# Kernel optimization log

Hardware: AMD Instinct MI355X
Metric: run time of the kernel (lower is better)

## Reference

```python
import jax, jax.numpy as jnp
import numpy as np

B, N, E = 4, 1024, 8192
NF_IN, NF_H, NF_OUT = 32, 128, 3


def _lin(key, fan_in, fan_out):
    k1, k2 = jax.random.split(key)
    bound = 1.0 / np.sqrt(fan_in)
    W = jax.random.uniform(k1, (fan_in, fan_out), jnp.float32, -bound, bound)
    b = jax.random.uniform(k2, (fan_out,), jnp.float32, -bound, bound)
    return W, b


def setup_inputs() -> dict:
    key = jax.random.key(0)
    ks = jax.random.split(key, 16)
    x = jax.random.normal(ks[0], (B, N, NF_IN), jnp.float32)
    # One-hot receiver/sender relation matrices [B, E, N]
    recv = jax.random.randint(ks[1], (B, E), 0, N)
    send = jax.random.randint(ks[2], (B, E), 0, N)
    Rr = jax.nn.one_hot(recv, N, dtype=jnp.float32)
    Rs = jax.nn.one_hot(send, N, dtype=jnp.float32)
    neW0, neb0 = _lin(ks[3], NF_IN, NF_H)
    neW1, neb1 = _lin(ks[4], NF_H, NF_H)
    neW2, neb2 = _lin(ks[5], NF_H, NF_H)
    eeW0, eeb0 = _lin(ks[6], NF_IN * 2, NF_H)
    eeW1, eeb1 = _lin(ks[7], NF_H, NF_H)
    eeW2, eeb2 = _lin(ks[8], NF_H, NF_H)
    npW, npb = _lin(ks[9], NF_H * 2, NF_H)
    epW, epb = _lin(ks[10], NF_H * 3, NF_H)
    ppW0, ppb0 = _lin(ks[11], NF_H * 2, NF_H)
    ppW1, ppb1 = _lin(ks[12], NF_H, NF_H)
    ppW2, ppb2 = _lin(ks[13], NF_H, NF_OUT)
    return dict(x=x, Rr=Rr, Rs=Rs, pstep=2,
                neW0=neW0, neb0=neb0, neW1=neW1, neb1=neb1, neW2=neW2, neb2=neb2,
                eeW0=eeW0, eeb0=eeb0, eeW1=eeW1, eeb1=eeb1, eeW2=eeW2, eeb2=eeb2,
                npW=npW, npb=npb, epW=epW, epb=epb,
                ppW0=ppW0, ppb0=ppb0, ppW1=ppW1, ppb1=ppb1, ppW2=ppW2, ppb2=ppb2)


def _encoder(x, W0, b0, W1, b1, W2, b2):
    # Linear->ReLU x3 (ReLU after last layer too)
    h = jax.nn.relu(x @ W0 + b0)
    h = jax.nn.relu(h @ W1 + b1)
    return jax.nn.relu(h @ W2 + b2)


def _predictor(x, W0, b0, W1, b1, W2, b2):
    h = jax.nn.relu(x @ W0 + b0)
    h = jax.nn.relu(h @ W1 + b1)
    return h @ W2 + b2


def reference(x, Rr, Rs, pstep,
              neW0, neb0, neW1, neb1, neW2, neb2,
              eeW0, eeb0, eeW1, eeb1, eeW2, eeb2,
              npW, npb, epW, epb,
              ppW0, ppb0, ppW1, ppb1, ppW2, ppb2):
    node_encode = _encoder(x, neW0, neb0, neW1, neb1, neW2, neb2)  # [B,N,H]
    node_effect = node_encode
    x_r = jnp.einsum('ben,bnf->bef', Rr, x)  # gather receiver features
    x_s = jnp.einsum('ben,bnf->bef', Rs, x)  # gather sender features
    edge_encode = _encoder(jnp.concatenate([x_r, x_s], -1),
                           eeW0, eeb0, eeW1, eeb1, eeW2, eeb2)  # [B,E,H]
    for _ in range(pstep):
        ne_r = jnp.einsum('ben,bnh->beh', Rr, node_effect)
        ne_s = jnp.einsum('ben,bnh->beh', Rs, node_effect)
        edge_in = jnp.concatenate([edge_encode, ne_r, ne_s], -1)  # [B,E,3H]
        edge_effect = jax.nn.relu(edge_in @ epW + epb)  # [B,E,H]
        agg = jnp.einsum('ben,beh->bnh', Rr, edge_effect)  # scatter-add to receivers
        node_in = jnp.concatenate([node_encode, agg], -1)  # [B,N,2H]
        node_effect = jax.nn.relu(node_in @ npW + npb + node_effect)  # residual
    node_reps = _predictor(jnp.concatenate([node_encode, node_effect], -1),
                           ppW0, ppb0, ppW1, ppb1, ppW2, ppb2)  # [B,N,out]
    return node_reps
```

## Files before the change

kernel.cpp:

```cpp
#include <hip/hip_runtime.h>
#include <hip/hip_bf16.h>


typedef unsigned short u16;
typedef __attribute__((ext_vector_type(8))) __bf16 bf16x8;
typedef __attribute__((ext_vector_type(4))) float f32x4;

#define N_    1024
#define BN    4096
#define BE    32768
#define LOG_E 13
#define H_    128
#define LSTR  132

__device__ __forceinline__ u16 f2bf(float f) {
    __bf16 h = (__bf16)f;
    return __builtin_bit_cast(u16, h);
}

__device__ __forceinline__ bf16x8 cvt8(float4 f0, float4 f1) {
    bf16x8 a;
    a[0] = (__bf16)f0.x; a[1] = (__bf16)f0.y; a[2] = (__bf16)f0.z; a[3] = (__bf16)f0.w;
    a[4] = (__bf16)f1.x; a[5] = (__bf16)f1.y; a[6] = (__bf16)f1.z; a[7] = (__bf16)f1.w;
    return a;
}

__device__ __forceinline__ bf16x8 a_from_f32(const float* p) {
    float4 f0 = *(const float4*)p;
    float4 f1 = *(const float4*)(p + 4);
    return cvt8(f0, f1);
}

__device__ __forceinline__ bf16x8 a_from_lds(const float* lds, int r, int quad, int c) {
    return a_from_f32(lds + r * LSTR + c * 32 + quad * 8);
}

__device__ __forceinline__ void mm8(const u16* __restrict__ Wf, int c, bf16x8 a,
                                    f32x4* acc, int lane) {
    const u16* wp = Wf + ((size_t)c * 8) * 64 * 8;
    #pragma unroll
    for (int nt = 0; nt < 8; ++nt) {
        bf16x8 bw = *(const bf16x8*)(wp + (size_t)(nt * 64 + lane) * 8);
        acc[nt] = __builtin_amdgcn_mfma_f32_16x16x32_bf16(a, bw, acc[nt], 0, 0, 0);
    }
}

__device__ __forceinline__ void mm4(const u16* __restrict__ Wf, int c, int ntb,
                                    bf16x8 a, f32x4* acc, int lane) {
    const u16* wp = Wf + ((size_t)c * 8) * 64 * 8;
    #pragma unroll
    for (int nt = 0; nt < 4; ++nt) {
        bf16x8 bw = *(const bf16x8*)(wp + (size_t)((ntb + nt) * 64 + lane) * 8);
        acc[nt] = __builtin_amdgcn_mfma_f32_16x16x32_bf16(a, bw, acc[nt], 0, 0, 0);
    }
}

__device__ __forceinline__ void mm2(const u16* __restrict__ Wf, int c, int ntb,
                                    bf16x8 a, f32x4* acc, int lane) {
    const u16* wp = Wf + ((size_t)c * 8) * 64 * 8;
    #pragma unroll
    for (int nt = 0; nt < 2; ++nt) {
        bf16x8 bw = *(const bf16x8*)(wp + (size_t)((ntb + nt) * 64 + lane) * 8);
        acc[nt] = __builtin_amdgcn_mfma_f32_16x16x32_bf16(a, bw, acc[nt], 0, 0, 0);
    }
}

__device__ __forceinline__ void zacc8(f32x4* acc) {
    #pragma unroll
    for (int t = 0; t < 8; ++t) acc[t] = (f32x4){0.f, 0.f, 0.f, 0.f};
}
__device__ __forceinline__ void zacc4(f32x4* acc) {
    #pragma unroll
    for (int t = 0; t < 4; ++t) acc[t] = (f32x4){0.f, 0.f, 0.f, 0.f};
}

__device__ __forceinline__ void epi8_lds(float* lds, const f32x4* acc,
                                         const float* __restrict__ bias,
                                         int quad, int m) {
    #pragma unroll
    for (int nt = 0; nt < 8; ++nt) {
        float bv = bias[nt * 16 + m];
        #pragma unroll
        for (int i = 0; i < 4; ++i)
            lds[(quad * 4 + i) * LSTR + nt * 16 + m] = fmaxf(acc[nt][i] + bv, 0.f);
    }
}

__device__ __forceinline__ void epi4_lds(float* lds, const f32x4* acc,
                                         const float* __restrict__ bias,
                                         int quad, int m, int ntb) {
    #pragma unroll
    for (int nt = 0; nt < 4; ++nt) {
        int col = (ntb + nt) * 16 + m;
        float bv = bias[col];
        #pragma unroll
        for (int i = 0; i < 4; ++i)
            lds[(quad * 4 + i) * LSTR + col] = fmaxf(acc[nt][i] + bv, 0.f);
    }
}

struct WDesc { const float* src; u16* dst; int K; };
struct WPack { WDesc d[10]; };

__global__ __launch_bounds__(256) void k_wprep(WPack P, float* __restrict__ agg) {
    if (blockIdx.y == 10) {
        int i = blockIdx.x * 256 + threadIdx.x;
        for (int t = i; t < BN * H_ / 4; t += 192 * 256)
            ((float4*)agg)[t] = make_float4(0.f, 0.f, 0.f, 0.f);
        return;
    }
    WDesc d = P.d[blockIdx.y];
    int i = blockIdx.x * 256 + threadIdx.x;
    if (i >= d.K * 128) return;
    int j    = i & 7;
    int lane = (i >> 3) & 63;
    int nt   = (i >> 9) & 7;
    int c    = i >> 12;
    int k = c * 32 + (lane >> 4) * 8 + j;
    int n = nt * 16 + (lane & 15);
    d.dst[i] = f2bf(d.src[k * 128 + n]);
}

__global__ __launch_bounds__(256) void k_extract(const float* __restrict__ Rr,
                                                 const float* __restrict__ Rs,
                                                 int* __restrict__ recv,
                                                 int* __restrict__ send) {
    int wave = threadIdx.x >> 6, lane = threadIdx.x & 63;
    int g = blockIdx.x * 4 + wave;
    const float* src;
    int* dst;
    if (g < BE) { src = Rr + (size_t)g * N_;        dst = recv + g; }
    else        { src = Rs + (size_t)(g - BE) * N_; dst = send + (g - BE); }
    int idx = 0;
    bool done = false;
    #pragma unroll
    for (int it = 0; it < 4; ++it) {
        if (!done) {
            int base = it * 256 + lane * 4;
            float4 v = *(const float4*)(src + base);
            int found = -1;
            if      (v.x != 0.f) found = base;
            else if (v.y != 0.f) found = base + 1;
            else if (v.z != 0.f) found = base + 2;
            else if (v.w != 0.f) found = base + 3;
            unsigned long long msk = __ballot(found >= 0);
            if (msk) {
                int sl = __ffsll((long long)msk) - 1;
                idx = __shfl(found, sl, 64);
                done = true;
            }
        }
    }
    if (lane == 0) *dst = idx;
}

__global__ __launch_bounds__(128) void k_node3(
    const float* __restrict__ x,
    const u16* __restrict__ W0, const float* __restrict__ b0,
    const u16* __restrict__ W1, const float* __restrict__ b1,
    const u16* __restrict__ W2, const float* __restrict__ b2,
    float* __restrict__ nenc_f, u16* __restrict__ nenc_bf)
{
    __shared__ float lds[2][16 * LSTR];
    int tid = threadIdx.x, lane = tid & 63, w = tid >> 6;
    int m = lane & 15, quad = lane >> 4;
    int row16 = blockIdx.x * 16, ntb = w * 4;
    f32x4 acc[4];

    zacc4(acc);
    mm4(W0, 0, ntb, a_from_f32(x + (size_t)(row16 + m) * 32 + quad * 8), acc, lane);
    epi4_lds(lds[0], acc, b0, quad, m, ntb);
    __syncthreads();

    zacc4(acc);
    #pragma unroll
    for (int c = 0; c < 4; ++c) mm4(W1, c, ntb, a_from_lds(lds[0], m, quad, c), acc, lane);
    epi4_lds(lds[1], acc, b1, quad, m, ntb);
    __syncthreads();

    zacc4(acc);
    #pragma unroll
    for (int c = 0; c < 4; ++c) mm4(W2, c, ntb, a_from_lds(lds[1], m, quad, c), acc, lane);
    epi4_lds(lds[0], acc, b2, quad, m, ntb);
    __syncthreads();

    #pragma unroll
    for (int t = 0; t < 16; ++t) {
        int flat = t * 128 + tid, r = flat >> 7, col = flat & 127;
        nenc_f[(size_t)(row16 + r) * H_ + col] = lds[0][r * LSTR + col];
    }
    #pragma unroll
    for (int t = 0; t < 8; ++t) {
        int p = t * 128 + tid, r = p >> 6, c2 = (p & 63) * 2;
        u16 lo = f2bf(lds[0][r * LSTR + c2]);
        u16 hi = f2bf(lds[0][r * LSTR + c2 + 1]);
        *(unsigned*)(nenc_bf + (size_t)(row16 + r) * H_ + c2) =
            (unsigned)lo | ((unsigned)hi << 16);
    }
}

__global__ __launch_bounds__(64) void k_edge3(
    const float* __restrict__ x,
    const int* __restrict__ recv, const int* __restrict__ send,
    const u16* __restrict__ W0, const float* __restrict__ b0,
    const u16* __restrict__ W1, const float* __restrict__ b1,
    const u16* __restrict__ W2, const float* __restrict__ b2,
    u16* __restrict__ eenc)
{
    __shared__ float lds[2][16 * LSTR];
    int lane = threadIdx.x, m = lane & 15, quad = lane >> 4;
    int row16 = blockIdx.x * 16;
    int e = row16 + m, b = e >> LOG_E;
    long rr = (long)b * N_ + recv[e];
    long rs = (long)b * N_ + send[e];
    f32x4 acc[8];

    zacc8(acc);
    mm8(W0, 0, a_from_f32(x + rr * 32 + quad * 8), acc, lane);
    mm8(W0, 1, a_from_f32(x + rs * 32 + quad * 8), acc, lane);
    epi8_lds(lds[0], acc, b0, quad, m);

    zacc8(acc);
    #pragma unroll
    for (int c = 0; c < 4; ++c) mm8(W1, c, a_from_lds(lds[0], m, quad, c), acc, lane);
    epi8_lds(lds[1], acc, b1, quad, m);

    zacc8(acc);
    #pragma unroll
    for (int c = 0; c < 4; ++c) mm8(W2, c, a_from_lds(lds[1], m, quad, c), acc, lane);
    epi8_lds(lds[0], acc, b2, quad, m);

    #pragma unroll
    for (int t = 0; t < 16; ++t) {
        int col = lane * 2;
        u16 lo = f2bf(lds[0][t * LSTR + col]);
        u16 hi = f2bf(lds[0][t * LSTR + col + 1]);
        *(unsigned*)(eenc + (size_t)(row16 + t) * H_ + col) =
            (unsigned)lo | ((unsigned)hi << 16);
    }
}

__global__ __launch_bounds__(64) void k_eprop(
    const u16* __restrict__ eenc, const u16* __restrict__ eff_bf,
    const int* __restrict__ recv, const int* __restrict__ send,
    const u16* __restrict__ Wf, const float* __restrict__ bias,
    float* __restrict__ agg)
{
    int lane = threadIdx.x, m = lane & 15, quad = lane >> 4;
    int row16 = blockIdx.x * 16;
    int e = row16 + m;
    long rr = ((long)(e >> LOG_E) * N_ + recv[e]) * H_;
    long rs = ((long)(e >> LOG_E) * N_ + send[e]) * H_;
    f32x4 acc[8];
    zacc8(acc);

    #pragma unroll
    for (int c = 0; c < 4; ++c)
        mm8(Wf, c, *(const bf16x8*)(eenc + (size_t)e * H_ + c * 32 + quad * 8), acc, lane);
    #pragma unroll
    for (int c = 0; c < 4; ++c)
        mm8(Wf, 4 + c, *(const bf16x8*)(eff_bf + rr + c * 32 + quad * 8), acc, lane);
    #pragma unroll
    for (int c = 0; c < 4; ++c)
        mm8(Wf, 8 + c, *(const bf16x8*)(eff_bf + rs + c * 32 + quad * 8), acc, lane);

    size_t tgt[4];
    #pragma unroll
    for (int i = 0; i < 4; ++i) {
        int r = row16 + quad * 4 + i;
        tgt[i] = ((size_t)(r >> LOG_E) * N_ + recv[r]) * H_;
    }
    #pragma unroll
    for (int nt = 0; nt < 8; ++nt) {
        int col = nt * 16 + m;
        float bv = bias[col];
        #pragma unroll
        for (int i = 0; i < 4; ++i)
            atomicAdd(agg + tgt[i] + col, fmaxf(acc[nt][i] + bv, 0.f));
    }
}

__global__ __launch_bounds__(256) void k_nprop(
    const u16* __restrict__ nenc_bf, float* __restrict__ agg,
    const float* __restrict__ eff_f,
    const u16* __restrict__ Wf, const float* __restrict__ bias,
    float* __restrict__ nout_f, u16* __restrict__ nout_bf)
{
    int tid = threadIdx.x, lane = tid & 63, w = tid >> 6;
    int m = lane & 15, quad = lane >> 4;
    int row16 = blockIdx.x * 16, row = row16 + m, ntb = w * 2;
    f32x4 acc[2];
    acc[0] = (f32x4){0.f, 0.f, 0.f, 0.f};
    acc[1] = (f32x4){0.f, 0.f, 0.f, 0.f};

    #pragma unroll
    for (int c = 0; c < 4; ++c)
        mm2(Wf, c, ntb,
            *(const bf16x8*)(nenc_bf + (size_t)row * H_ + c * 32 + quad * 8), acc, lane);
    #pragma unroll
    for (int c = 0; c < 4; ++c)
        mm2(Wf, 4 + c, ntb,
            a_from_f32(agg + (size_t)row * H_ + c * 32 + quad * 8), acc, lane);

    __syncthreads();

    #pragma unroll
    for (int nt = 0; nt < 2; ++nt) {
        int col = (ntb + nt) * 16 + m;
        float bv = bias[col];
        #pragma unroll
        for (int i = 0; i < 4; ++i) {
            int r = row16 + quad * 4 + i;
            float v = fmaxf(acc[nt][i] + bv + eff_f[(size_t)r * H_ + col], 0.f);
            nout_f[(size_t)r * H_ + col] = v;
            nout_bf[(size_t)r * H_ + col] = f2bf(v);
            agg[(size_t)r * H_ + col] = 0.f;
        }
    }
}

__global__ __launch_bounds__(128) void k_pred(
    const u16* __restrict__ nenc_bf, const u16* __restrict__ eff_bf,
    const u16* __restrict__ W0, const float* __restrict__ b0,
    const u16* __restrict__ W1, const float* __restrict__ b1,
    const float* __restrict__ W2, const float* __restrict__ b2,
    float* __restrict__ out)
{
    __shared__ float lds[2][16 * LSTR];
    int tid = threadIdx.x, lane = tid & 63, w = tid >> 6;
    int m = lane & 15, quad = lane >> 4;
    int row16 = blockIdx.x * 16, row = row16 + m, ntb = w * 4;
    f32x4 acc[4];

    zacc4(acc);
    #pragma unroll
    for (int c = 0; c < 4; ++c)
        mm4(W0, c, ntb,
            *(const bf16x8*)(nenc_bf + (size_t)row * H_ + c * 32 + quad * 8), acc, lane);
    #pragma unroll
    for (int c = 0; c < 4; ++c)
        mm4(W0, 4 + c, ntb,
            *(const bf16x8*)(eff_bf + (size_t)row * H_ + c * 32 + quad * 8), acc, lane);
    epi4_lds(lds[0], acc, b0, quad, m, ntb);
    __syncthreads();

    zacc4(acc);
    #pragma unroll
    for (int c = 0; c < 4; ++c) mm4(W1, c, ntb, a_from_lds(lds[0], m, quad, c), acc, lane);
    epi4_lds(lds[1], acc, b1, quad, m, ntb);
    __syncthreads();

    if (w == 0) {
        int r = lane & 15, col = lane >> 4;
        if (col < 3) {
            float s = 0.f;
            #pragma unroll 8
            for (int k = 0; k < 128; ++k)
                s += lds[1][r * LSTR + k] * W2[k * 3 + col];
            out[(size_t)(row16 + r) * 3 + col] = s + b2[col];
        }
    }
}

extern "C" void kernel_launch(void* const* d_in, const int* in_sizes, int n_in,
                              void* d_out, int out_size, void* d_ws, size_t ws_size,
                              hipStream_t stream) {
    (void)in_sizes; (void)n_in; (void)out_size; (void)ws_size;

    const float* x    = (const float*)d_in[0];
    const float* Rr   = (const float*)d_in[1];
    const float* Rs   = (const float*)d_in[2];
    const float* neW0 = (const float*)d_in[4];  const float* neb0 = (const float*)d_in[5];
    const float* neW1 = (const float*)d_in[6];  const float* neb1 = (const float*)d_in[7];
    const float* neW2 = (const float*)d_in[8];  const float* neb2 = (const float*)d_in[9];
    const float* eeW0 = (const float*)d_in[10]; const float* eeb0 = (const float*)d_in[11];
    const float* eeW1 = (const float*)d_in[12]; const float* eeb1 = (const float*)d_in[13];
    const float* eeW2 = (const float*)d_in[14]; const float* eeb2 = (const float*)d_in[15];
    const float* npW  = (const float*)d_in[16]; const float* npb  = (const float*)d_in[17];
    const float* epW  = (const float*)d_in[18]; const float* epb  = (const float*)d_in[19];
    const float* ppW0 = (const float*)d_in[20]; const float* ppb0 = (const float*)d_in[21];
    const float* ppW1 = (const float*)d_in[22]; const float* ppb1 = (const float*)d_in[23];
    const float* ppW2 = (const float*)d_in[24]; const float* ppb2 = (const float*)d_in[25];

    char* ws = (char*)d_ws;
    size_t off = 0;
    auto alloc = [&](size_t bytes) -> char* {
        char* p = ws + off;
        off += (bytes + 255) & ~(size_t)255;
        return p;
    };

    u16* f_neW0 = (u16*)alloc(32  * 128 * 2);
    u16* f_neW1 = (u16*)alloc(128 * 128 * 2);
    u16* f_neW2 = (u16*)alloc(128 * 128 * 2);
    u16* f_eeW0 = (u16*)alloc(64  * 128 * 2);
    u16* f_eeW1 = (u16*)alloc(128 * 128 * 2);
    u16* f_eeW2 = (u16*)alloc(128 * 128 * 2);
    u16* f_epW  = (u16*)alloc(384 * 128 * 2);
    u16* f_npW  = (u16*)alloc(256 * 128 * 2);
    u16* f_ppW0 = (u16*)alloc(256 * 128 * 2);
    u16* f_ppW1 = (u16*)alloc(128 * 128 * 2);
    int*   recv = (int*)alloc(BE * 4);
    int*   send = (int*)alloc(BE * 4);
    float* nenc_f  = (float*)alloc((size_t)BN * H_ * 4);
    u16*   nenc_bf = (u16*)alloc((size_t)BN * H_ * 2);
    float* nef1_f  = (float*)alloc((size_t)BN * H_ * 4);
    u16*   nef1_bf = (u16*)alloc((size_t)BN * H_ * 2);
    float* nef2_f  = (float*)alloc((size_t)BN * H_ * 4);
    u16*   nef2_bf = (u16*)alloc((size_t)BN * H_ * 2);
    float* agg  = (float*)alloc((size_t)BN * H_ * 4);
    u16*   eenc = (u16*)alloc((size_t)BE * H_ * 2);

    WPack P;
    P.d[0] = {neW0, f_neW0, 32};
    P.d[1] = {neW1, f_neW1, 128};
    P.d[2] = {neW2, f_neW2, 128};
    P.d[3] = {eeW0, f_eeW0, 64};
    P.d[4] = {eeW1, f_eeW1, 128};
    P.d[5] = {eeW2, f_eeW2, 128};
    P.d[6] = {epW,  f_epW,  384};
    P.d[7] = {npW,  f_npW,  256};
    P.d[8] = {ppW0, f_ppW0, 256};
    P.d[9] = {ppW1, f_ppW1, 128};
    k_wprep<<<dim3(192, 11), 256, 0, stream>>>(P, agg);

    k_extract<<<(2 * BE) / 4, 256, 0, stream>>>(Rr, Rs, recv, send);

    k_node3<<<BN / 16, 128, 0, stream>>>(x, f_neW0, neb0, f_neW1, neb1, f_neW2, neb2,
                                         nenc_f, nenc_bf);
    k_edge3<<<BE / 16, 64, 0, stream>>>(x, recv, send,
                                        f_eeW0, eeb0, f_eeW1, eeb1, f_eeW2, eeb2, eenc);

    k_eprop<<<BE / 16, 64, 0, stream>>>(eenc, nenc_bf, recv, send, f_epW, epb, agg);
    k_nprop<<<BN / 16, 256, 0, stream>>>(nenc_bf, agg, nenc_f, f_npW, npb, nef1_f, nef1_bf);
    k_eprop<<<BE / 16, 64, 0, stream>>>(eenc, nef1_bf, recv, send, f_epW, epb, agg);
    k_nprop<<<BN / 16, 256, 0, stream>>>(nenc_bf, agg, nef1_f, f_npW, npb, nef2_f, nef2_bf);

    k_pred<<<BN / 16, 128, 0, stream>>>(nenc_bf, nef2_bf, f_ppW0, ppb0, f_ppW1, ppb1,
                                        ppW2, ppb2, (float*)d_out);
}
```

Measured before the change: 386.7 us.

## Replace atomic scatter-add with per-node edge lists and gather aggregation

```diff
diff --git a/kernel.cpp b/kernel.cpp
--- a/kernel.cpp
+++ b/kernel.cpp
@@ -12,6 +12,8 @@
 #define LOG_E 13
 #define H_    128
 #define LSTR  132
+#define ECAP  64
+#define ASTR  136
 
 __device__ __forceinline__ u16 f2bf(float f) {
     __bf16 h = (__bf16)f;
@@ -102,11 +104,10 @@
 struct WDesc { const float* src; u16* dst; int K; };
 struct WPack { WDesc d[10]; };
 
-__global__ __launch_bounds__(256) void k_wprep(WPack P, float* __restrict__ agg) {
+__global__ __launch_bounds__(256) void k_wprep(WPack P, int* __restrict__ deg) {
     if (blockIdx.y == 10) {
         int i = blockIdx.x * 256 + threadIdx.x;
-        for (int t = i; t < BN * H_ / 4; t += 192 * 256)
-            ((float4*)agg)[t] = make_float4(0.f, 0.f, 0.f, 0.f);
+        if (i < BN / 4) ((int4*)deg)[i] = make_int4(0, 0, 0, 0);
         return;
     }
     WDesc d = P.d[blockIdx.y];
@@ -124,7 +125,9 @@
 __global__ __launch_bounds__(256) void k_extract(const float* __restrict__ Rr,
                                                  const float* __restrict__ Rs,
                                                  int* __restrict__ recv,
-                                                 int* __restrict__ send) {
+                                                 int* __restrict__ send,
+                                                 int* __restrict__ deg,
+                                                 int* __restrict__ eidx) {
     int wave = threadIdx.x >> 6, lane = threadIdx.x & 63;
     int g = blockIdx.x * 4 + wave;
     const float* src;
@@ -151,7 +154,14 @@
             }
         }
     }
-    if (lane == 0) *dst = idx;
+    if (lane == 0) {
+        *dst = idx;
+        if (g < BE) {
+            int node = (g >> LOG_E) * N_ + idx;
+            int pos = atomicAdd(deg + node, 1);
+            if (pos < ECAP) eidx[node * ECAP + pos] = g;
+        }
+    }
 }
 
 __global__ __launch_bounds__(128) void k_node3(
@@ -244,7 +254,7 @@
     const u16* __restrict__ eenc, const u16* __restrict__ eff_bf,
     const int* __restrict__ recv, const int* __restrict__ send,
     const u16* __restrict__ Wf, const float* __restrict__ bias,
-    float* __restrict__ agg)
+    float* __restrict__ edge_eff)
 {
     int lane = threadIdx.x, m = lane & 15, quad = lane >> 4;
     int row16 = blockIdx.x * 16;
@@ -264,31 +274,71 @@
     for (int c = 0; c < 4; ++c)
         mm8(Wf, 8 + c, *(const bf16x8*)(eff_bf + rs + c * 32 + quad * 8), acc, lane);
 
-    size_t tgt[4];
-    #pragma unroll
-    for (int i = 0; i < 4; ++i) {
-        int r = row16 + quad * 4 + i;
-        tgt[i] = ((size_t)(r >> LOG_E) * N_ + recv[r]) * H_;
-    }
     #pragma unroll
     for (int nt = 0; nt < 8; ++nt) {
         int col = nt * 16 + m;
         float bv = bias[col];
         #pragma unroll
         for (int i = 0; i < 4; ++i)
-            atomicAdd(agg + tgt[i] + col, fmaxf(acc[nt][i] + bv, 0.f));
+            edge_eff[(size_t)(row16 + quad * 4 + i) * H_ + col] =
+                fmaxf(acc[nt][i] + bv, 0.f);
     }
 }
 
 __global__ __launch_bounds__(256) void k_nprop(
-    const u16* __restrict__ nenc_bf, float* __restrict__ agg,
+    const u16* __restrict__ nenc_bf, const float* __restrict__ edge_eff,
+    const int* __restrict__ deg, const int* __restrict__ eidx,
     const float* __restrict__ eff_f,
     const u16* __restrict__ Wf, const float* __restrict__ bias,
     float* __restrict__ nout_f, u16* __restrict__ nout_bf)
 {
+    __shared__ u16 aggl[16 * ASTR];
     int tid = threadIdx.x, lane = tid & 63, w = tid >> 6;
     int m = lane & 15, quad = lane >> 4;
-    int row16 = blockIdx.x * 16, row = row16 + m, ntb = w * 2;
+    int row16 = blockIdx.x * 16;
+
+    int nd = tid >> 4, l = tid & 15;
+    int node = row16 + nd;
+    int dg = deg[node]; dg = dg < ECAP ? dg : ECAP;
+    int ev = eidx[node * ECAP + l];
+    int base = lane & 48;
+    float s[8] = {0.f, 0.f, 0.f, 0.f, 0.f, 0.f, 0.f, 0.f};
+    int d16 = dg < 16 ? dg : 16;
+    int t = 0;
+    for (; t + 1 < d16; t += 2) {
+        int e0 = __shfl(ev, base | t, 64);
+        int e1 = __shfl(ev, base | (t + 1), 64);
+        const float* p0 = edge_eff + (size_t)e0 * H_ + l * 8;
+        const float* p1 = edge_eff + (size_t)e1 * H_ + l * 8;
+        float4 a0 = *(const float4*)p0, b0 = *(const float4*)(p0 + 4);
+        float4 a1 = *(const float4*)p1, b1 = *(const float4*)(p1 + 4);
+        s[0] += a0.x + a1.x; s[1] += a0.y + a1.y;
+        s[2] += a0.z + a1.z; s[3] += a0.w + a1.w;
+        s[4] += b0.x + b1.x; s[5] += b0.y + b1.y;
+        s[6] += b0.z + b1.z; s[7] += b0.w + b1.w;
+    }
+    if (t < d16) {
+        int e0 = __shfl(ev, base | t, 64);
+        const float* p0 = edge_eff + (size_t)e0 * H_ + l * 8;
+        float4 a0 = *(const float4*)p0, b0 = *(const float4*)(p0 + 4);
+        s[0] += a0.x; s[1] += a0.y; s[2] += a0.z; s[3] += a0.w;
+        s[4] += b0.x; s[5] += b0.y; s[6] += b0.z; s[7] += b0.w;
+        ++t;
+    }
+    for (; t < dg; ++t) {
+        int e0 = eidx[node * ECAP + t];
+        const float* p0 = edge_eff + (size_t)e0 * H_ + l * 8;
+        float4 a0 = *(const float4*)p0, b0 = *(const float4*)(p0 + 4);
+        s[0] += a0.x; s[1] += a0.y; s[2] += a0.z; s[3] += a0.w;
+        s[4] += b0.x; s[5] += b0.y; s[6] += b0.z; s[7] += b0.w;
+    }
+    bf16x8 o;
+    #pragma unroll
+    for (int j = 0; j < 8; ++j) o[j] = (__bf16)s[j];
+    *(bf16x8*)(aggl + nd * ASTR + l * 8) = o;
+    __syncthreads();
+
+    int row = row16 + m, ntb = w * 2;
     f32x4 acc[2];
     acc[0] = (f32x4){0.f, 0.f, 0.f, 0.f};
     acc[1] = (f32x4){0.f, 0.f, 0.f, 0.f};
@@ -300,9 +350,7 @@
     #pragma unroll
     for (int c = 0; c < 4; ++c)
         mm2(Wf, 4 + c, ntb,
-            a_from_f32(agg + (size_t)row * H_ + c * 32 + quad * 8), acc, lane);
-
-    __syncthreads();
+            *(const bf16x8*)(aggl + m * ASTR + c * 32 + quad * 8), acc, lane);
 
     #pragma unroll
     for (int nt = 0; nt < 2; ++nt) {
@@ -314,7 +362,6 @@
             float v = fmaxf(acc[nt][i] + bv + eff_f[(size_t)r * H_ + col], 0.f);
             nout_f[(size_t)r * H_ + col] = v;
             nout_bf[(size_t)r * H_ + col] = f2bf(v);
-            agg[(size_t)r * H_ + col] = 0.f;
         }
     }
 }
@@ -402,13 +449,15 @@
     u16* f_ppW1 = (u16*)alloc(128 * 128 * 2);
     int*   recv = (int*)alloc(BE * 4);
     int*   send = (int*)alloc(BE * 4);
+    int*   deg  = (int*)alloc(BN * 4);
+    int*   eidx = (int*)alloc((size_t)BN * ECAP * 4);
     float* nenc_f  = (float*)alloc((size_t)BN * H_ * 4);
     u16*   nenc_bf = (u16*)alloc((size_t)BN * H_ * 2);
     float* nef1_f  = (float*)alloc((size_t)BN * H_ * 4);
     u16*   nef1_bf = (u16*)alloc((size_t)BN * H_ * 2);
     float* nef2_f  = (float*)alloc((size_t)BN * H_ * 4);
     u16*   nef2_bf = (u16*)alloc((size_t)BN * H_ * 2);
-    float* agg  = (float*)alloc((size_t)BN * H_ * 4);
+    float* edge_eff = (float*)alloc((size_t)BE * H_ * 4);
     u16*   eenc = (u16*)alloc((size_t)BE * H_ * 2);
 
     WPack P;
@@ -422,19 +471,21 @@
     P.d[7] = {npW,  f_npW,  256};
     P.d[8] = {ppW0, f_ppW0, 256};
     P.d[9] = {ppW1, f_ppW1, 128};
-    k_wprep<<<dim3(192, 11), 256, 0, stream>>>(P, agg);
-
-    k_extract<<<(2 * BE) / 4, 256, 0, stream>>>(Rr, Rs, recv, send);
+    k_wprep<<<dim3(192, 11), 256, 0, stream>>>(P, deg);
+
+    k_extract<<<(2 * BE) / 4, 256, 0, stream>>>(Rr, Rs, recv, send, deg, eidx);
 
     k_node3<<<BN / 16, 128, 0, stream>>>(x, f_neW0, neb0, f_neW1, neb1, f_neW2, neb2,
                                          nenc_f, nenc_bf);
     k_edge3<<<BE / 16, 64, 0, stream>>>(x, recv, send,
                                         f_eeW0, eeb0, f_eeW1, eeb1, f_eeW2, eeb2, eenc);
 
-    k_eprop<<<BE / 16, 64, 0, stream>>>(eenc, nenc_bf, recv, send, f_epW, epb, agg);
-    k_nprop<<<BN / 16, 256, 0, stream>>>(nenc_bf, agg, nenc_f, f_npW, npb, nef1_f, nef1_bf);
-    k_eprop<<<BE / 16, 64, 0, stream>>>(eenc, nef1_bf, recv, send, f_epW, epb, agg);
-    k_nprop<<<BN / 16, 256, 0, stream>>>(nenc_bf, agg, nef1_f, f_npW, npb, nef2_f, nef2_bf);
+    k_eprop<<<BE / 16, 64, 0, stream>>>(eenc, nenc_bf, recv, send, f_epW, epb, edge_eff);
+    k_nprop<<<BN / 16, 256, 0, stream>>>(nenc_bf, edge_eff, deg, eidx, nenc_f,
+                                         f_npW, npb, nef1_f, nef1_bf);
+    k_eprop<<<BE / 16, 64, 0, stream>>>(eenc, nef1_bf, recv, send, f_epW, epb, edge_eff);
+    k_nprop<<<BN / 16, 256, 0, stream>>>(nenc_bf, edge_eff, deg, eidx, nef1_f,
+                                         f_npW, npb, nef2_f, nef2_bf);
 
     k_pred<<<BN / 16, 128, 0, stream>>>(nenc_bf, nef2_bf, f_ppW0, ppb0, f_ppW1, ppb1,
                                         ppW2, ppb2, (float*)d_out);
```

Result: faster. 375.5 us (-2.9%).
